# Kernel tuning notes

Hardware: AMD Instinct MI355X
Metric: run time of the kernel (lower is better)

Reference implementation:

```python
import jax, jax.numpy as jnp
import numpy as np

IN_FEATURES = 512
NUM_TREES = 512
DEPTH = 5
NLEAF = 2 ** DEPTH
RESPONSE_DIM = 1
BATCH = 2048


def make_path_map():
    # OBLIVIOUS_map from DeTree.InitPathWay: nodes[j] = j (oblivious tree),
    # index 2*node + bit into the flattened [depth, 2] choice tensor.
    path = []
    for no in range(NLEAF):
        b = no
        for j in range(DEPTH):
            path.append(2 * j + (b % 2))
            b //= 2
    return np.asarray(path, dtype=np.int32)  # [NLEAF * DEPTH]


def setup_inputs() -> dict:
    key = jax.random.key(0)
    k1, k2, k3, k4, k5 = jax.random.split(key, 5)
    x = jax.random.normal(k1, (BATCH, IN_FEATURES), dtype=jnp.float32)
    # nn.init.uniform_ on [in_features, num_trees * depth]
    feat_attention = jax.random.uniform(k2, (IN_FEATURES, NUM_TREES * DEPTH), dtype=jnp.float32)
    feature_thresholds = jax.random.normal(k3, (NUM_TREES, DEPTH), dtype=jnp.float32)
    log_temperatures = jax.random.normal(k4, (NUM_TREES, DEPTH), dtype=jnp.float32) * 0.1
    response = jax.random.normal(k5, (NUM_TREES, RESPONSE_DIM, NLEAF), dtype=jnp.float32)
    path_map = jnp.asarray(make_path_map())
    return {"x": x, "feat_attention": feat_attention,
            "feature_thresholds": feature_thresholds,
            "log_temperatures": log_temperatures,
            "response": response, "path_map": path_map}


def reference(x, feat_attention, feature_thresholds, log_temperatures, response, path_map):
    B, F = x.shape
    n, d = feature_thresholds.shape
    # feature gating: softmax over the feature axis (dim=0)
    choice_weight = jax.nn.softmax(feat_attention, axis=0).reshape(F, n, d)
    feature_values = jnp.einsum('bf,fnd->bnd', x, choice_weight)  # [B, n, d]
    # temperature-scaled split logits
    tl = (feature_values - feature_thresholds) * jnp.exp(-log_temperatures)
    logits = jnp.stack([-tl, tl], axis=-1)  # [B, n, d, 2]
    # sparsemoid binary gate
    choice = jnp.clip(0.5 * logits + 0.5, 0.0, 1.0)
    # route through tree paths: gather per-leaf path gates, product along depth
    gate = choice.reshape(B, n, d * 2)[:, :, path_map].reshape(B, n, -1, d)
    bins_prob = jnp.prod(gate, axis=-1)  # [B, n, nLeaf]
    out = jnp.einsum('bnl,ncl->bnc', bins_prob, response)  # [B, n, response_dim]
    return out.reshape(B, -1)  # flatten_output=True
```

## Files before the change

### kernel.cpp

```cpp
#include <hip/hip_runtime.h>
#include <hip/hip_bf16.h>

#define F_DIM 512
#define NT 512
#define DEPTH 5
#define NCOL (NT * DEPTH)
#define BATCH 2048

typedef __attribute__((ext_vector_type(8))) short bf16x8;
typedef __attribute__((ext_vector_type(4))) float f32x4;

__device__ __forceinline__ void gl2lds16(const void* g, void* l) {
    __builtin_amdgcn_global_load_lds((const __attribute__((address_space(1))) void*)g,
                                     (__attribute__((address_space(3))) void*)l,
                                     16, 0, 0);
}

__global__ __launch_bounds__(256) void prep(const float* __restrict__ x,
                                            const float* __restrict__ fa,
                                            __hip_bfloat16* __restrict__ Xb,
                                            __hip_bfloat16* __restrict__ Wt) {
    if (blockIdx.x < 1024) {
        const size_t i = (size_t)blockIdx.x * 256 + threadIdx.x;
        const float4 v = ((const float4*)x)[i];
        union { ushort4 u; __hip_bfloat16 h[4]; } pk;
        pk.h[0] = __float2bfloat16(v.x);
        pk.h[1] = __float2bfloat16(v.y);
        pk.h[2] = __float2bfloat16(v.z);
        pk.h[3] = __float2bfloat16(v.w);
        ((ushort4*)Xb)[i] = pk.u;
        return;
    }
    const int bx = blockIdx.x - 1024;
    const int l = threadIdx.x & 15;
    const int g = threadIdx.x >> 4;
    const int col = bx * 16 + l;
    const int f0 = g * 32;
    __shared__ float red[16][16];

    float e[32];
    float s = 0.f;
#pragma unroll
    for (int i = 0; i < 32; ++i) {
        e[i] = __expf(fa[(size_t)(f0 + i) * NCOL + col]);
        s += e[i];
    }
    red[g][l] = s;
    __syncthreads();

    float S = 0.f;
#pragma unroll
    for (int gg = 0; gg < 16; ++gg) S += red[gg][l];
    const float inv = 1.0f / S;

    __hip_bfloat16* dst = Wt + (size_t)col * F_DIM + f0;
#pragma unroll
    for (int i = 0; i < 32; i += 4) {
        union { ushort4 u; __hip_bfloat16 h[4]; } pk;
#pragma unroll
        for (int jj = 0; jj < 4; ++jj)
            pk.h[jj] = __float2bfloat16(e[i + jj] * inv);
        *(ushort4*)(dst + i) = pk.u;
    }
}

__global__ __launch_bounds__(256, 1) void gemm_tree(const __hip_bfloat16* __restrict__ A,
                                                    const __hip_bfloat16* __restrict__ Bt,
                                                    const float* __restrict__ th,
                                                    const float* __restrict__ lt,
                                                    const float* __restrict__ resp,
                                                    float* __restrict__ out) {
    __shared__ __align__(16) char smem[36864];
    __hip_bfloat16* As = (__hip_bfloat16*)smem;
    __hip_bfloat16* Bs = (__hip_bfloat16*)(smem + 16384);
    float* E = (float*)smem;

    const int tid = threadIdx.x;
    const int w = tid >> 6;
    const int l = tid & 63;
    const int m0 = blockIdx.y * 128;
    const int n0c = blockIdx.x * 160;
    const int n0t = blockIdx.x * 32;
    const int wm = (w & 1) * 64;
    const int wn = (w >> 1) * 80;

    f32x4 acc[4][5] = {};

    const int srow = l >> 3;
    const int schunk = (l & 7) ^ srow;

    for (int kt = 0; kt < 8; ++kt) {
        const int k0 = kt * 64;
#pragma unroll
        for (int q = 0; q < 4; ++q) {
            const int g = q * 4 + w;
            gl2lds16(A + ((size_t)(m0 + g * 8 + srow) * F_DIM + k0 + schunk * 8),
                     As + g * 8 * 64);
        }
#pragma unroll
        for (int q = 0; q < 5; ++q) {
            const int g = q * 4 + w;
            gl2lds16(Bt + ((size_t)(n0c + g * 8 + srow) * F_DIM + k0 + schunk * 8),
                     Bs + g * 8 * 64);
        }
        __syncthreads();

#pragma unroll
        for (int ks = 0; ks < 2; ++ks) {
            bf16x8 af[4], bfr[5];
            const int cb = ks * 4 + (l >> 4);
#pragma unroll
            for (int im = 0; im < 4; ++im) {
                const int r = wm + im * 16 + (l & 15);
                af[im] = *(const bf16x8*)(As + r * 64 + ((cb ^ (r & 7)) * 8));
            }
#pragma unroll
            for (int in = 0; in < 5; ++in) {
                const int r = wn + in * 16 + (l & 15);
                bfr[in] = *(const bf16x8*)(Bs + r * 64 + ((cb ^ (r & 7)) * 8));
            }
#pragma unroll
            for (int im = 0; im < 4; ++im)
#pragma unroll
                for (int in = 0; in < 5; ++in)
                    acc[im][in] = __builtin_amdgcn_mfma_f32_16x16x32_bf16(
                        af[im], bfr[in], acc[im][in], 0, 0, 0);
        }
        __syncthreads();
    }

    const int tree = tid & 31;
    const int rg = tid >> 5;
    const int gt = n0t + tree;

    float al[DEPTH], be[DEPTH];
#pragma unroll
    for (int j = 0; j < DEPTH; ++j) {
        const float a = 0.5f * __expf(-lt[gt * DEPTH + j]);
        al[j] = a;
        be[j] = 0.5f - th[gt * DEPTH + j] * a;
    }
    float rs[32];
#pragma unroll
    for (int i = 0; i < 32; ++i) rs[i] = resp[gt * 32 + i];

    const int PAD = 161;
#pragma unroll
    for (int im = 0; im < 4; ++im) {
#pragma unroll
        for (int in = 0; in < 5; ++in) {
            const int scol = wn + in * 16 + (l & 15);
#pragma unroll
            for (int r = 0; r < 4; ++r) {
                const int sr = (w & 1) * 16 + (l >> 4) * 4 + r;
                E[sr * PAD + scol] = acc[im][in][r];
            }
        }
        __syncthreads();

#pragma unroll
        for (int rr = 0; rr < 4; ++rr) {
            const int s = rg * 4 + rr;
            const int gb = m0 + ((s < 16) ? (im * 16 + s) : (64 + im * 16 + (s - 16)));
            const float* f = E + s * PAD + tree * 5;
            float c1[DEPTH];
#pragma unroll
            for (int j = 0; j < DEPTH; ++j) {
                const float v = fmaf(al[j], f[j], be[j]);
                c1[j] = fminf(fmaxf(v, 0.f), 1.f);
            }
            float s16[16], s8[8], s4[4], s2[2];
#pragma unroll
            for (int m = 0; m < 16; ++m) s16[m] = fmaf(c1[0], rs[2*m+1] - rs[2*m], rs[2*m]);
#pragma unroll
            for (int m = 0; m < 8; ++m)  s8[m]  = fmaf(c1[1], s16[2*m+1] - s16[2*m], s16[2*m]);
#pragma unroll
            for (int m = 0; m < 4; ++m)  s4[m]  = fmaf(c1[2], s8[2*m+1] - s8[2*m], s8[2*m]);
#pragma unroll
            for (int m = 0; m < 2; ++m)  s2[m]  = fmaf(c1[3], s4[2*m+1] - s4[2*m], s4[2*m]);
            out[(size_t)gb * NT + gt] = fmaf(c1[4], s2[1] - s2[0], s2[0]);
        }
        __syncthreads();
    }
}

extern "C" void kernel_launch(void* const* d_in, const int* in_sizes, int n_in,
                              void* d_out, int out_size, void* d_ws, size_t ws_size,
                              hipStream_t stream) {
    const float* x    = (const float*)d_in[0];
    const float* fa   = (const float*)d_in[1];
    const float* th   = (const float*)d_in[2];
    const float* lt   = (const float*)d_in[3];
    const float* resp = (const float*)d_in[4];

    char* ws = (char*)d_ws;
    __hip_bfloat16* Wt = (__hip_bfloat16*)(ws);
    __hip_bfloat16* Xb = (__hip_bfloat16*)(ws + (4u << 20));
    float* out = (float*)d_out;

    hipLaunchKernelGGL(prep, dim3(1024 + 160), dim3(256), 0, stream, x, fa, Xb, Wt);
    hipLaunchKernelGGL(gemm_tree, dim3(NCOL / 160, BATCH / 128), dim3(256), 0, stream,
                       Xb, Wt, th, lt, resp, out);
}
```

Before: 88.11 us.

## Double-buffer B tiles in LDS and load A fragments directly from global

The GEMM main loop now double-buffers only the B (weight) tile in LDS, issuing the next stage's global-to-LDS loads before computing the current one, so one barrier per iteration replaces two. The A (activation) fragments are read straight from global memory into registers instead of being staged through LDS. This aims to overlap B loads with MFMA work and cut LDS traffic and barriers. In exchange, A reads become per-wave global loads that are redundant across the waves sharing the same rows and are exposed to latency without prefetching, and the block uses more LDS.

```diff
diff --git a/kernel.cpp b/kernel.cpp
--- a/kernel.cpp
+++ b/kernel.cpp
@@ -70,9 +70,9 @@
                                                     const float* __restrict__ lt,
                                                     const float* __restrict__ resp,
                                                     float* __restrict__ out) {
-    __shared__ __align__(16) char smem[36864];
-    __hip_bfloat16* As = (__hip_bfloat16*)smem;
-    __hip_bfloat16* Bs = (__hip_bfloat16*)(smem + 16384);
+    __shared__ __align__(16) char smem[40960];
+    __hip_bfloat16* Bs0 = (__hip_bfloat16*)smem;
+    __hip_bfloat16* Bs1 = (__hip_bfloat16*)(smem + 20480);
     float* E = (float*)smem;
 
     const int tid = threadIdx.x;
@@ -89,45 +89,52 @@
     const int srow = l >> 3;
     const int schunk = (l & 7) ^ srow;
 
-    for (int kt = 0; kt < 8; ++kt) {
-        const int k0 = kt * 64;
-#pragma unroll
-        for (int q = 0; q < 4; ++q) {
-            const int g = q * 4 + w;
-            gl2lds16(A + ((size_t)(m0 + g * 8 + srow) * F_DIM + k0 + schunk * 8),
-                     As + g * 8 * 64);
-        }
+    auto stageB = [&](int st, __hip_bfloat16* buf) {
+        const int k0 = st * 64;
 #pragma unroll
         for (int q = 0; q < 5; ++q) {
             const int g = q * 4 + w;
             gl2lds16(Bt + ((size_t)(n0c + g * 8 + srow) * F_DIM + k0 + schunk * 8),
-                     Bs + g * 8 * 64);
-        }
+                     buf + g * 8 * 64);
+        }
+    };
+
+    stageB(0, Bs0);
+
+    for (int st = 0; st < 8; ++st) {
+        __hip_bfloat16* cur = (st & 1) ? Bs1 : Bs0;
+        __hip_bfloat16* nxt = (st & 1) ? Bs0 : Bs1;
         __syncthreads();
-
+        if (st < 7) stageB(st + 1, nxt);
+
+        const int k0 = st * 64;
+        bf16x8 af[2][4];
 #pragma unroll
         for (int ks = 0; ks < 2; ++ks) {
-            bf16x8 af[4], bfr[5];
             const int cb = ks * 4 + (l >> 4);
 #pragma unroll
-            for (int im = 0; im < 4; ++im) {
-                const int r = wm + im * 16 + (l & 15);
-                af[im] = *(const bf16x8*)(As + r * 64 + ((cb ^ (r & 7)) * 8));
-            }
+            for (int im = 0; im < 4; ++im)
+                af[ks][im] = *(const bf16x8*)(
+                    A + (size_t)(m0 + wm + im * 16 + (l & 15)) * F_DIM + k0 + cb * 8);
+        }
+#pragma unroll
+        for (int ks = 0; ks < 2; ++ks) {
+            const int cb = ks * 4 + (l >> 4);
+            bf16x8 bfr[5];
 #pragma unroll
             for (int in = 0; in < 5; ++in) {
                 const int r = wn + in * 16 + (l & 15);
-                bfr[in] = *(const bf16x8*)(Bs + r * 64 + ((cb ^ (r & 7)) * 8));
+                bfr[in] = *(const bf16x8*)(cur + r * 64 + ((cb ^ (r & 7)) * 8));
             }
 #pragma unroll
             for (int im = 0; im < 4; ++im)
 #pragma unroll
                 for (int in = 0; in < 5; ++in)
                     acc[im][in] = __builtin_amdgcn_mfma_f32_16x16x32_bf16(
-                        af[im], bfr[in], acc[im][in], 0, 0, 0);
-        }
-        __syncthreads();
-    }
+                        af[ks][im], bfr[in], acc[im][in], 0, 0, 0);
+        }
+    }
+    __syncthreads();
 
     const int tree = tid & 31;
     const int rg = tid >> 5;
```

Result: slower. 93.32 us (+5.9%).
